# Kernel tuning notes

Hardware: AMD Instinct MI355X
Metric: run time of the kernel (lower is better)

Reference implementation:

```python
import jax, jax.numpy as jnp
import numpy as np

NA = 3            # anchor_num
NC = 80           # cls_num
IGNORE = 0.5      # ignore_threshold
OBJ_SCALE = 1.0
NOOBJ_SCALE = 100.0
ANCHORS = jnp.array([[0.05, 0.07], [0.12, 0.16], [0.28, 0.35]], dtype=jnp.float32)


def setup_inputs() -> dict:
    key = jax.random.key(0)
    k1, k2, k3, k4, k5 = jax.random.split(key, 5)
    out = jax.random.normal(k1, (16, NA * (NC + 5), 52, 52), dtype=jnp.float32)
    nGts = 240
    b = jax.random.randint(k2, (nGts,), 0, 16).astype(jnp.float32)
    lab = jax.random.randint(k3, (nGts,), 0, NC).astype(jnp.float32)
    xy = jax.random.uniform(k4, (nGts, 2), minval=0.02, maxval=0.98)
    wh = jax.random.uniform(k5, (nGts, 2), minval=0.02, maxval=0.6)
    gts = jnp.concatenate([b[:, None], lab[:, None], xy, wh], axis=1).astype(jnp.float32)
    return {"out": out, "gts": gts}


def _build_targets(gts, nB, nG):
    # gts: [nGts, 6] = (batch, label, cx, cy, w, h), normalized coords
    gx, gy, gw, gh = gts[:, 2], gts[:, 3], gts[:, 4], gts[:, 5]
    aw = ANCHORS[:, 0][:, None]  # [nA,1]
    ah = ANCHORS[:, 1][:, None]
    # iou_wo_center: boxes share center -> overlap of w/h
    inter = jnp.minimum(gw[None, :], aw) * jnp.minimum(gh[None, :], ah)
    ious = inter / (gw[None, :] * gh[None, :] + aw * ah - inter)  # [nA, nGts]
    best_n = jnp.argmax(ious, axis=0)                              # [nGts]
    batch = gts[:, 0].astype(jnp.int32)
    labels = gts[:, 1].astype(jnp.int32)
    gi = (nG * gx).astype(jnp.int32)
    gj = (nG * gy).astype(jnp.int32)

    obj = jnp.zeros((nB, NA, nG, nG), bool).at[batch, best_n, gj, gi].set(True)
    # noobj: 1 everywhere, zero at best anchor and wherever anchor IoU > ignore thres
    keep = (ious.T <= IGNORE).astype(jnp.int32)                    # [nGts, nA]
    anc = jnp.arange(NA, dtype=jnp.int32)
    noobj = jnp.ones((nB, NA, nG, nG), jnp.int32)
    noobj = noobj.at[batch[:, None], anc[None, :], gj[:, None], gi[:, None]].min(keep)
    noobj = noobj.at[batch, best_n, gj, gi].set(0).astype(bool)

    tb = jnp.zeros((nB, NA, nG, nG, 4), jnp.float32)
    tb = tb.at[batch, best_n, gj, gi].set(jnp.stack([gx, gy, gw, gh], axis=1))
    tcls = jnp.zeros((nB, NA, nG, nG, NC), jnp.float32)
    tcls = tcls.at[batch, best_n, gj, gi, labels].set(1.0)
    return obj, noobj, tb, tcls


def _masked_mean(x, m):
    mf = m.astype(x.dtype)
    return jnp.sum(x * mf) / jnp.maximum(jnp.sum(mf), 1.0)


def _bce(p, t, m):
    # torch BCELoss clamps log terms at -100
    logp = jnp.clip(jnp.log(p), -100.0, None)
    log1mp = jnp.clip(jnp.log1p(-p), -100.0, None)
    return _masked_mean(-(t * logp + (1.0 - t) * log1mp), m)


def _forward(out, gts):
    nB, _, nG, _ = out.shape
    pred = out.reshape(nB, NA, NC + 5, nG, nG).transpose(0, 1, 3, 4, 2)  # [B,A,G,G,5+C]
    xs = jax.nn.sigmoid(pred[..., 0])
    ys = jax.nn.sigmoid(pred[..., 1])
    ws = pred[..., 2]
    hs = pred[..., 3]
    conf = jax.nn.sigmoid(pred[..., 4])
    cls_s = jax.nn.sigmoid(pred[..., 5:])
    # NOTE: pd_bboxes in the original is computed but only its SHAPE is used in
    # build_target during training, so it is dead compute and omitted here.

    obj, noobj, tb, tcls = _build_targets(gts, nB, nG)

    aw = ANCHORS[:, 0].reshape(1, NA, 1, 1)
    ah = ANCHORS[:, 1].reshape(1, NA, 1, 1)
    gxs = tb[..., 0] * nG
    gys = tb[..., 1] * nG
    txs = gxs - jnp.floor(gxs)
    tys = gys - jnp.floor(gys)
    tws = jnp.where(obj, tb[..., 2] / aw, 1.0)  # safe log outside mask
    ths = jnp.where(obj, tb[..., 3] / ah, 1.0)

    loss_xy = _masked_mean((xs - txs) ** 2, obj) + _masked_mean((ys - tys) ** 2, obj)
    loss_wh = _masked_mean((ws - jnp.log(tws)) ** 2, obj) + _masked_mean((hs - jnp.log(ths)) ** 2, obj)

    tconf = obj.astype(jnp.float32)
    loss_conf = OBJ_SCALE * _bce(conf, tconf, obj) + NOOBJ_SCALE * _bce(conf, tconf, noobj)

    mb = jnp.broadcast_to(obj[..., None], cls_s.shape)
    loss_cls = _bce(cls_s, tcls, mb)
    return loss_xy + loss_wh + loss_conf + loss_cls


def reference(out, gts):
    return _forward(out, gts)
```

## Files before the change

### kernel.cpp

```cpp
#include <hip/hip_runtime.h>
#include <math.h>

#define NA 3
#define NC 80
#define NCH 85
#define NG 52
#define NGG (NG * NG)
#define MAXG 256
#define HSZ 512
#define NCONF_V (NGG / 4)
#define BLKT 256
#define MAGIC 0x5EEDC0DEu
#define L2E 1.44269504088896340736f
#define LN2 0.69314718055994530942f

__device__ __forceinline__ float hw_exp2(float x) { return __builtin_amdgcn_exp2f(x); }
__device__ __forceinline__ float hw_log2(float x) { return __builtin_amdgcn_logf(x); }

__device__ __forceinline__ float softplus_clip(float z) {
    float sp = fmaxf(z, 0.0f) + LN2 * hw_log2(1.0f + hw_exp2(-fabsf(z) * L2E));
    return fminf(sp, 100.0f);
}

__device__ __forceinline__ float sigmoid_fast(float p) {
    return 1.0f / (1.0f + hw_exp2(-p * L2E));
}

__global__ __launch_bounds__(BLKT, 1)
void yolo_loss_kernel(const float* __restrict__ out, const float* __restrict__ gts,
                      float* __restrict__ loss_out, unsigned* __restrict__ ws,
                      int nGts, int nB, int nconfv) {
    __shared__ int h_key[HSZ], h_min[HSZ], h_mask[HSZ];
    __shared__ int h_max[HSZ][NA];
    __shared__ int s_base[MAXG], s_coff[MAXG], s_lab[MAXG], s_clr[MAXG];
    __shared__ float s_txs[MAXG], s_tys[MAXG], s_ltw[MAXG], s_lth[MAXG];
    __shared__ unsigned char s_oo[MAXG];
    __shared__ int s_cnt[2];
    __shared__ float s_wred[BLKT / 64];

    const float AW[NA] = {0.05f, 0.12f, 0.28f};
    const float AH[NA] = {0.07f, 0.16f, 0.35f};
    const int t = threadIdx.x;

    for (int i = t; i < HSZ; i += BLKT) {
        h_key[i] = -1; h_min[i] = 0x7fffffff; h_mask[i] = 0;
        h_max[i][0] = -1; h_max[i][1] = -1; h_max[i][2] = -1;
    }
    if (t < 2) s_cnt[t] = 0;
    __syncthreads();

    int slot = -1, bn = 0;
    if (t < nGts) {
        float gx = gts[t * 6 + 2], gy = gts[t * 6 + 3];
        float gw = gts[t * 6 + 4], gh = gts[t * 6 + 5];
        int b = (int)gts[t * 6 + 0];
        s_lab[t] = (int)gts[t * 6 + 1];
        int gi = (int)((float)NG * gx), gj = (int)((float)NG * gy);
        int mask = 0; float best = -1.0f;
        for (int a = 0; a < NA; ++a) {
            float inter = fminf(gw, AW[a]) * fminf(gh, AH[a]);
            float iou = inter / (gw * gh + AW[a] * AH[a] - inter);
            if (iou > 0.5f) mask |= 1 << a;
            if (iou > best) { best = iou; bn = a; }
        }
        mask |= 1 << bn;

        int key = (b * NG + gj) * NG + gi;
        slot = (int)(((unsigned)key * 2654435761u) >> 23) & (HSZ - 1);
        for (;;) {
            int prev = atomicCAS(&h_key[slot], -1, key);
            if (prev == -1 || prev == key) break;
            slot = (slot + 1) & (HSZ - 1);
        }
        atomicMin(&h_min[slot], t);
        atomicMax(&h_max[slot][bn], t);
        atomicOr(&h_mask[slot], mask);

        s_base[t] = ((b * NA + bn) * NCH) * NGG + gj * NG + gi;
        s_coff[t] = (b * NA * NCH + 4) * NGG + gj * NG + gi;
        float gxs = (float)NG * gx; s_txs[t] = gxs - floorf(gxs);
        float gys = (float)NG * gy; s_tys[t] = gys - floorf(gys);
        s_ltw[t] = logf(gw / AW[bn]);
        s_lth[t] = logf(gh / AH[bn]);
    }
    __syncthreads();
    if (t < nGts) {
        bool oo = (h_max[slot][bn] == t);
        s_oo[t] = oo ? 1 : 0;
        if (oo) atomicAdd(&s_cnt[0], 1);
        int cm = (h_min[slot] == t) ? h_mask[slot] : 0;
        s_clr[t] = cm;
        if (cm) atomicAdd(&s_cnt[1], __popc(cm));
    }
    __syncthreads();

    const int nObj = s_cnt[0], nClr = s_cnt[1];
    const float invObj = 1.0f / fmaxf((float)nObj, 1.0f);
    const float wNoobj = 100.0f / fmaxf((float)(nB * NA * NGG - nClr), 1.0f);
    const float invCls = 1.0f / fmaxf((float)nObj * (float)NC, 1.0f);

    float conf_sum = 0.0f, obj_sum = 0.0f, cls_sum = 0.0f, clr_sum = 0.0f;

    const int work = nconfv + nGts * NCH + nGts * NA;
    const int n = blockIdx.x * BLKT + t;
    if (n < work) {
        if (n < nconfv) {
            int plane = n / NCONF_V, q = n - plane * NCONF_V;
            const float4 v = *(const float4*)(out + (plane * NCH + 4) * NGG + q * 4);
            float m = fmaxf(v.x, 0.0f) + fmaxf(v.y, 0.0f) + fmaxf(v.z, 0.0f) + fmaxf(v.w, 0.0f);
            float p = (1.0f + hw_exp2(-fabsf(v.x) * L2E)) * (1.0f + hw_exp2(-fabsf(v.y) * L2E))
                    * (1.0f + hw_exp2(-fabsf(v.z) * L2E)) * (1.0f + hw_exp2(-fabsf(v.w) * L2E));
            conf_sum = m + LN2 * hw_log2(p);
        } else {
            int m = n - nconfv;
            if (m < nGts * NCH) {
                unsigned g = (unsigned)m / NCH;
                unsigned c = (unsigned)m - g * NCH;
                if (s_oo[g]) {
                    int base = s_base[g];
                    if (c == 0) {
                        float d = sigmoid_fast(out[base]) - s_txs[g]; obj_sum = d * d;
                    } else if (c == 1) {
                        float d = sigmoid_fast(out[base + NGG]) - s_tys[g]; obj_sum = d * d;
                    } else if (c == 2) {
                        float d = out[base + 2 * NGG] - s_ltw[g]; obj_sum = d * d;
                    } else if (c == 3) {
                        float d = out[base + 3 * NGG] - s_lth[g]; obj_sum = d * d;
                    } else if (c == 4) {
                        obj_sum = softplus_clip(-out[base + 4 * NGG]);
                    } else {
                        int cc = (int)c - 5;
                        float w = out[base + (5 + cc) * NGG];
                        cls_sum = softplus_clip(cc == s_lab[g] ? -w : w);
                    }
                }
            } else {
                int k = m - nGts * NCH;
                int g = k / NA, a = k - g * NA;
                if ((s_clr[g] >> a) & 1)
                    clr_sum = softplus_clip(out[s_coff[g] + a * (NCH * NGG)]);
            }
        }
    }

    float partial = invObj * obj_sum + invCls * cls_sum + wNoobj * (conf_sum - clr_sum);
    for (int o = 32; o > 0; o >>= 1) partial += __shfl_down(partial, o);
    if ((t & 63) == 0) s_wred[t >> 6] = partial;
    __syncthreads();

    if (t == 0) {
        float p = s_wred[0] + s_wred[1] + s_wred[2] + s_wred[3];
        unsigned bits = __float_as_uint(p);
        __hip_atomic_store(&ws[2 * blockIdx.x], bits,
                           __ATOMIC_RELAXED, __HIP_MEMORY_SCOPE_AGENT);
        __hip_atomic_store(&ws[2 * blockIdx.x + 1], bits ^ MAGIC,
                           __ATOMIC_RELEASE, __HIP_MEMORY_SCOPE_AGENT);
    }

    if (blockIdx.x == 0 && t < 64) {
        float v = 0.0f;
        const int nblk = (int)gridDim.x;
        for (int sIdx = t; sIdx < nblk; sIdx += 64) {
            unsigned c, s;
            do {
                c = __hip_atomic_load(&ws[2 * sIdx + 1], __ATOMIC_ACQUIRE, __HIP_MEMORY_SCOPE_AGENT);
                s = __hip_atomic_load(&ws[2 * sIdx],     __ATOMIC_RELAXED, __HIP_MEMORY_SCOPE_AGENT);
            } while ((c ^ MAGIC) != s);
            v += __uint_as_float(s);
        }
        for (int o = 32; o > 0; o >>= 1) v += __shfl_down(v, o);
        if (t == 0) loss_out[0] = v;
    }
}

extern "C" void kernel_launch(void* const* d_in, const int* in_sizes, int n_in,
                              void* d_out, int out_size, void* d_ws, size_t ws_size,
                              hipStream_t stream) {
    const float* out = (const float*)d_in[0];
    const float* gts = (const float*)d_in[1];
    int nGts = in_sizes[1] / 6;
    if (nGts > MAXG) nGts = MAXG;
    int nB = in_sizes[0] / (NA * NCH * NGG);
    int nconfv = nB * NA * NCONF_V;

    int work = nconfv + nGts * NCH + nGts * NA;
    int nblk = (work + BLKT - 1) / BLKT;

    yolo_loss_kernel<<<nblk, BLKT, 0, stream>>>(out, gts, (float*)d_out, (unsigned*)d_ws,
                                                nGts, nB, nconfv);
}
```

Measured before the change: 13.65 us.

## Issue global loads before the shared-memory hash build to overlap latency

Each thread now computes its own work-item addresses from gts directly and issues its global load of `out` (float4 conf or scalar gather) before the block-wide hash-table construction and barriers. The per-GT shared arrays for base offsets and targets are removed, and targets are recomputed per thread. This is meant to hide global memory latency behind the setup phase instead of serializing load after it. The cost is redundant per-thread recomputation of IoU/targets, extra gts reads, and unconditional loads even for GTs that turn out not to be the owning object.

```diff
diff --git a/kernel.cpp b/kernel.cpp
--- a/kernel.cpp
+++ b/kernel.cpp
@@ -32,15 +32,58 @@
                       int nGts, int nB, int nconfv) {
     __shared__ int h_key[HSZ], h_min[HSZ], h_mask[HSZ];
     __shared__ int h_max[HSZ][NA];
-    __shared__ int s_base[MAXG], s_coff[MAXG], s_lab[MAXG], s_clr[MAXG];
-    __shared__ float s_txs[MAXG], s_tys[MAXG], s_ltw[MAXG], s_lth[MAXG];
     __shared__ unsigned char s_oo[MAXG];
+    __shared__ int s_clr[MAXG];
     __shared__ int s_cnt[2];
     __shared__ float s_wred[BLKT / 64];
 
     const float AW[NA] = {0.05f, 0.12f, 0.28f};
     const float AH[NA] = {0.07f, 0.16f, 0.35f};
     const int t = threadIdx.x;
+    const int n = blockIdx.x * BLKT + t;
+    const int work = nconfv + nGts * NCH + nGts * NA;
+
+    float4 v4 = make_float4(0.f, 0.f, 0.f, 0.f);
+    float loaded = 0.f, tgt = 0.f;
+    int region = -1, cc = 0, aa = 0, lab2 = 0;
+    unsigned g = 0;
+    if (n < work) {
+        if (n < nconfv) {
+            region = 0;
+            int plane = n / NCONF_V, q = n - plane * NCONF_V;
+            v4 = *(const float4*)(out + (plane * NCH + 4) * NGG + q * 4);
+        } else {
+            int m = n - nconfv;
+            if (m < nGts * NCH) {
+                region = 1;
+                g = (unsigned)m / NCH; cc = m - (int)g * NCH;
+                float gx = gts[g * 6 + 2], gy = gts[g * 6 + 3];
+                float gw = gts[g * 6 + 4], gh = gts[g * 6 + 5];
+                int b = (int)gts[g * 6 + 0]; lab2 = (int)gts[g * 6 + 1];
+                int gi = (int)((float)NG * gx), gj = (int)((float)NG * gy);
+                float best = -1.f; int bn2 = 0;
+                for (int a = 0; a < NA; ++a) {
+                    float inter = fminf(gw, AW[a]) * fminf(gh, AH[a]);
+                    float iou = inter / (gw * gh + AW[a] * AH[a] - inter);
+                    if (iou > best) { best = iou; bn2 = a; }
+                }
+                int base = ((b * NA + bn2) * NCH) * NGG + gj * NG + gi;
+                loaded = out[base + cc * NGG];
+                if (cc == 0)      { float gxs = (float)NG * gx; tgt = gxs - floorf(gxs); }
+                else if (cc == 1) { float gys = (float)NG * gy; tgt = gys - floorf(gys); }
+                else if (cc == 2) tgt = logf(gw / AW[bn2]);
+                else if (cc == 3) tgt = logf(gh / AH[bn2]);
+            } else {
+                region = 2;
+                int k = m - nGts * NCH;
+                g = (unsigned)k / NA; aa = k - (int)g * NA;
+                float gx = gts[g * 6 + 2], gy = gts[g * 6 + 3];
+                int b = (int)gts[g * 6 + 0];
+                int gi = (int)((float)NG * gx), gj = (int)((float)NG * gy);
+                loaded = out[((b * NA + aa) * NCH + 4) * NGG + gj * NG + gi];
+            }
+        }
+    }
 
     for (int i = t; i < HSZ; i += BLKT) {
         h_key[i] = -1; h_min[i] = 0x7fffffff; h_mask[i] = 0;
@@ -54,9 +97,8 @@
         float gx = gts[t * 6 + 2], gy = gts[t * 6 + 3];
         float gw = gts[t * 6 + 4], gh = gts[t * 6 + 5];
         int b = (int)gts[t * 6 + 0];
-        s_lab[t] = (int)gts[t * 6 + 1];
         int gi = (int)((float)NG * gx), gj = (int)((float)NG * gy);
-        int mask = 0; float best = -1.0f;
+        int mask = 0; float best = -1.f;
         for (int a = 0; a < NA; ++a) {
             float inter = fminf(gw, AW[a]) * fminf(gh, AH[a]);
             float iou = inter / (gw * gh + AW[a] * AH[a] - inter);
@@ -75,13 +117,6 @@
         atomicMin(&h_min[slot], t);
         atomicMax(&h_max[slot][bn], t);
         atomicOr(&h_mask[slot], mask);
-
-        s_base[t] = ((b * NA + bn) * NCH) * NGG + gj * NG + gi;
-        s_coff[t] = (b * NA * NCH + 4) * NGG + gj * NG + gi;
-        float gxs = (float)NG * gx; s_txs[t] = gxs - floorf(gxs);
-        float gys = (float)NG * gy; s_tys[t] = gys - floorf(gys);
-        s_ltw[t] = logf(gw / AW[bn]);
-        s_lth[t] = logf(gh / AH[bn]);
     }
     __syncthreads();
     if (t < nGts) {
@@ -95,52 +130,25 @@
     __syncthreads();
 
     const int nObj = s_cnt[0], nClr = s_cnt[1];
-    const float invObj = 1.0f / fmaxf((float)nObj, 1.0f);
-    const float wNoobj = 100.0f / fmaxf((float)(nB * NA * NGG - nClr), 1.0f);
-    const float invCls = 1.0f / fmaxf((float)nObj * (float)NC, 1.0f);
+    const float invObj = 1.f / fmaxf((float)nObj, 1.f);
+    const float wNoobj = 100.f / fmaxf((float)(nB * NA * NGG - nClr), 1.f);
+    const float invCls = 1.f / fmaxf((float)nObj * (float)NC, 1.f);
 
-    float conf_sum = 0.0f, obj_sum = 0.0f, cls_sum = 0.0f, clr_sum = 0.0f;
-
-    const int work = nconfv + nGts * NCH + nGts * NA;
-    const int n = blockIdx.x * BLKT + t;
-    if (n < work) {
-        if (n < nconfv) {
-            int plane = n / NCONF_V, q = n - plane * NCONF_V;
-            const float4 v = *(const float4*)(out + (plane * NCH + 4) * NGG + q * 4);
-            float m = fmaxf(v.x, 0.0f) + fmaxf(v.y, 0.0f) + fmaxf(v.z, 0.0f) + fmaxf(v.w, 0.0f);
-            float p = (1.0f + hw_exp2(-fabsf(v.x) * L2E)) * (1.0f + hw_exp2(-fabsf(v.y) * L2E))
-                    * (1.0f + hw_exp2(-fabsf(v.z) * L2E)) * (1.0f + hw_exp2(-fabsf(v.w) * L2E));
-            conf_sum = m + LN2 * hw_log2(p);
-        } else {
-            int m = n - nconfv;
-            if (m < nGts * NCH) {
-                unsigned g = (unsigned)m / NCH;
-                unsigned c = (unsigned)m - g * NCH;
-                if (s_oo[g]) {
-                    int base = s_base[g];
-                    if (c == 0) {
-                        float d = sigmoid_fast(out[base]) - s_txs[g]; obj_sum = d * d;
-                    } else if (c == 1) {
-                        float d = sigmoid_fast(out[base + NGG]) - s_tys[g]; obj_sum = d * d;
-                    } else if (c == 2) {
-                        float d = out[base + 2 * NGG] - s_ltw[g]; obj_sum = d * d;
-                    } else if (c == 3) {
-                        float d = out[base + 3 * NGG] - s_lth[g]; obj_sum = d * d;
-                    } else if (c == 4) {
-                        obj_sum = softplus_clip(-out[base + 4 * NGG]);
-                    } else {
-                        int cc = (int)c - 5;
-                        float w = out[base + (5 + cc) * NGG];
-                        cls_sum = softplus_clip(cc == s_lab[g] ? -w : w);
-                    }
-                }
-            } else {
-                int k = m - nGts * NCH;
-                int g = k / NA, a = k - g * NA;
-                if ((s_clr[g] >> a) & 1)
-                    clr_sum = softplus_clip(out[s_coff[g] + a * (NCH * NGG)]);
-            }
+    float conf_sum = 0.f, obj_sum = 0.f, cls_sum = 0.f, clr_sum = 0.f;
+    if (region == 0) {
+        float m = fmaxf(v4.x, 0.f) + fmaxf(v4.y, 0.f) + fmaxf(v4.z, 0.f) + fmaxf(v4.w, 0.f);
+        float p = (1.f + hw_exp2(-fabsf(v4.x) * L2E)) * (1.f + hw_exp2(-fabsf(v4.y) * L2E))
+                * (1.f + hw_exp2(-fabsf(v4.z) * L2E)) * (1.f + hw_exp2(-fabsf(v4.w) * L2E));
+        conf_sum = m + LN2 * hw_log2(p);
+    } else if (region == 1) {
+        if (s_oo[g]) {
+            if (cc == 0 || cc == 1)      { float d = sigmoid_fast(loaded) - tgt; obj_sum = d * d; }
+            else if (cc == 2 || cc == 3) { float d = loaded - tgt; obj_sum = d * d; }
+            else if (cc == 4)            { obj_sum = softplus_clip(-loaded); }
+            else  cls_sum = softplus_clip((cc - 5) == lab2 ? -loaded : loaded);
         }
+    } else if (region == 2) {
+        if ((s_clr[g] >> aa) & 1) clr_sum = softplus_clip(loaded);
     }
 
     float partial = invObj * obj_sum + invCls * cls_sum + wNoobj * (conf_sum - clr_sum);
@@ -158,7 +166,7 @@
     }
 
     if (blockIdx.x == 0 && t < 64) {
-        float v = 0.0f;
+        float v = 0.f;
         const int nblk = (int)gridDim.x;
         for (int sIdx = t; sIdx < nblk; sIdx += 64) {
             unsigned c, s;
```

Measured after the change: 13.04 us. -4.5%, faster.
